# Kernel optimization log

Measured on AMD Instinct MI355X. Metric: run time of the kernel, lower is better.

The kernel has to match this reference:

```python
import jax, jax.numpy as jnp
import numpy as np

N_NODES = 10000
N_EDGES = 320000
D_NODE = 128
D_EDGE = 32
D_IN = 2 * D_NODE + D_EDGE  # 288, concat(sender, receiver, edge)
D_HID = 192                 # AutoMLP log-spaced hidden dim between 288 and 128
D_OUT = 128


def setup_inputs() -> dict:
    key = jax.random.key(0)
    ks = jax.random.split(key, 8)
    n_embed = jax.random.normal(ks[0], (N_NODES, D_NODE), dtype=jnp.float32)
    e_embed = jax.random.normal(ks[1], (N_EDGES, D_EDGE), dtype=jnp.float32)
    senders = jnp.sort(jax.random.randint(ks[2], (N_EDGES,), 0, N_NODES, dtype=jnp.int32))
    receivers = jax.random.randint(ks[3], (N_EDGES,), 0, N_NODES, dtype=jnp.int32)
    # AutoMLP parameters (lecun_normal-style scaling)
    W1 = jax.random.normal(ks[4], (D_IN, D_HID), dtype=jnp.float32) / np.sqrt(D_IN)
    b1 = jnp.zeros((D_HID,), dtype=jnp.float32)
    W2 = jax.random.normal(ks[5], (D_HID, D_OUT), dtype=jnp.float32) / np.sqrt(D_HID)
    b2 = jnp.zeros((D_OUT,), dtype=jnp.float32)
    return {"n_embed": n_embed, "e_embed": e_embed, "senders": senders,
            "receivers": receivers, "W1": W1, "b1": b1, "W2": W2, "b2": b2}


def reference(n_embed, e_embed, senders, receivers, W1, b1, W2, b2):
    # gather sender/receiver node embeddings and concat with edge features: [E, 288]
    inp = jnp.concatenate([n_embed[senders], n_embed[receivers], e_embed], axis=-1)
    # AutoMLP: Dense -> tanh -> Dense (final layer linear)
    h = jnp.tanh(inp @ W1 + b1)          # [E, 192]
    msg = h @ W2 + b2                    # [E, 128]
    # segment_mean over senders (sorted), num_segments = n_nodes
    seg_sum = jax.ops.segment_sum(msg, senders, num_segments=N_NODES,
                                  indices_are_sorted=True)
    counts = jax.ops.segment_sum(jnp.ones((msg.shape[0],), dtype=msg.dtype), senders,
                                 num_segments=N_NODES, indices_are_sorted=True)
    return seg_sum / jnp.maximum(counts, 1.0)[:, None]
```

## Files before the change

kernel.cpp:

```cpp
#include <hip/hip_runtime.h>

#define E_TOT 320000
#define NN    10000
#define DN    128
#define DE    32
#define DH    192
#define DO    128
#define EB    64
#define SHS   196

typedef __attribute__((ext_vector_type(8))) short bf16x8;
typedef __attribute__((ext_vector_type(4))) float f32x4;

#define W1_FRAGS (8*12*64)
#define E_FRAGS  (12*64)
#define W2_FRAGS (6*8*64)
#define FRAGS_TOT (W1_FRAGS + E_FRAGS + W2_FRAGS)
#define ZH (NN * DH / 4)
__device__ __align__(16) unsigned short g_p1[W1_FRAGS * 8];
__device__ __align__(16) unsigned short g_e [E_FRAGS * 8];
__device__ __align__(16) unsigned short g_p2[W2_FRAGS * 8];

__device__ __forceinline__ unsigned short f2bf(float f) {
    union { float f; unsigned u; } v; v.f = f;
    return (unsigned short)((v.u + 0x7FFFu + ((v.u >> 16) & 1u)) >> 16);
}
__device__ __forceinline__ float bflo(unsigned u) {
    union { unsigned v; float f; } t; t.v = u << 16; return t.f;
}
__device__ __forceinline__ float bfhi(unsigned u) {
    union { unsigned v; float f; } t; t.v = u & 0xFFFF0000u; return t.f;
}
__device__ __forceinline__ float bf2f(unsigned short s) {
    union { unsigned v; float f; } t; t.v = (unsigned)s << 16; return t.f;
}
__device__ __forceinline__ float tanh_fast(float x) {
    float ex = __expf(x + x);
    return 1.0f - 2.0f * __builtin_amdgcn_rcpf(ex + 1.0f);
}
__device__ __forceinline__ unsigned cvt_pk_bf16(float lo, float hi) {
    unsigned r;
    asm("v_cvt_pk_bf16_f32 %0, %1, %2" : "=v"(r) : "v"(lo), "v"(hi));
    return r;
}

__global__ void prep(const float* __restrict__ W1, const float* __restrict__ W2,
                     const int* __restrict__ senders,
                     float* __restrict__ Hbar, int* __restrict__ row_start)
{
    int f = blockIdx.x * 256 + threadIdx.x;
    unsigned short tmp[8];
    if (f < W1_FRAGS) {
        int kk = f / (12 * 64), nt = (f >> 6) % 12, lane = f & 63;
        int r0 = kk * 32 + ((lane >> 4) << 3);
        int c  = nt * 16 + (lane & 15);
        #pragma unroll
        for (int i = 0; i < 8; ++i) tmp[i] = f2bf(W1[(r0 + i) * DH + c]);
        *(uint4*)(g_p1 + (size_t)f * 8) = *(const uint4*)tmp;
    } else if (f < W1_FRAGS + E_FRAGS) {
        int f2 = f - W1_FRAGS;
        int mt = f2 >> 6, lane = f2 & 63;
        int k0 = ((lane >> 4) << 3);
        int hid = mt * 16 + (lane & 15);
        #pragma unroll
        for (int i = 0; i < 8; ++i) tmp[i] = f2bf(W1[(256 + k0 + i) * DH + hid]);
        *(uint4*)(g_e + (size_t)f2 * 8) = *(const uint4*)tmp;
    } else if (f < FRAGS_TOT) {
        int f3 = f - W1_FRAGS - E_FRAGS;
        int kk = f3 / (8 * 64), nt = (f3 >> 6) % 8, lane = f3 & 63;
        int r0 = kk * 32 + ((lane >> 4) << 3);
        int c  = nt * 16 + (lane & 15);
        #pragma unroll
        for (int i = 0; i < 8; ++i) tmp[i] = f2bf(W2[(r0 + i) * DO + c]);
        *(uint4*)(g_p2 + (size_t)f3 * 8) = *(const uint4*)tmp;
    } else if (f < FRAGS_TOT + ZH) {
        ((float4*)Hbar)[f - FRAGS_TOT] = make_float4(0.f, 0.f, 0.f, 0.f);
    } else if (f < FRAGS_TOT + ZH + E_TOT) {
        int e = f - FRAGS_TOT - ZH;
        int s_cur  = senders[e];
        int s_prev = (e == 0) ? -1 : senders[e - 1];
        if (s_prev != s_cur)
            for (int n = s_prev + 1; n <= s_cur; ++n) row_start[n] = e;
        if (e == E_TOT - 1)
            for (int n = s_cur + 1; n <= NN; ++n) row_start[n] = E_TOT;
    }
}

__global__ __launch_bounds__(256) void node_proj(
    const float* __restrict__ n_embed, const float* __restrict__ b1,
    unsigned short* __restrict__ P)
{
    __shared__ __align__(16) unsigned short s_a[64][136];
    const int tid  = threadIdx.x;
    const int half = blockIdx.y;
    const int n0   = blockIdx.x * 64;

    #pragma unroll
    for (int it = 0; it < 8; ++it) {
        int idx = tid + it * 256;
        int row = idx >> 5, c = idx & 31;
        float4 v = make_float4(0.f, 0.f, 0.f, 0.f);
        if (n0 + row < NN) v = ((const float4*)(n_embed + (size_t)(n0 + row) * DN))[c];
        unsigned t0 = cvt_pk_bf16(v.x, v.y), t1 = cvt_pk_bf16(v.z, v.w);
        *(uint2*)&s_a[row][c * 4] = make_uint2(t0, t1);
    }
    __syncthreads();

    const int lane = tid & 63, w = tid >> 6;
    const int arow = lane & 15, akb = (lane >> 4) * 8, rbase = (lane >> 4) * 4;

    f32x4 acc[4][3];
    #pragma unroll
    for (int mt = 0; mt < 4; ++mt)
        #pragma unroll
        for (int j = 0; j < 3; ++j) acc[mt][j] = (f32x4){0.f, 0.f, 0.f, 0.f};

    for (int kk = 0; kk < 4; ++kk) {
        bf16x8 a[4], b[3];
        #pragma unroll
        for (int mt = 0; mt < 4; ++mt)
            a[mt] = *(const bf16x8*)&s_a[mt * 16 + arow][kk * 32 + akb];
        #pragma unroll
        for (int j = 0; j < 3; ++j)
            b[j] = *(const bf16x8*)(g_p1 + (((size_t)(kk + 4 * half) * 12 + (3 * w + j)) * 64 + lane) * 8);
        #pragma unroll
        for (int mt = 0; mt < 4; ++mt)
            #pragma unroll
            for (int j = 0; j < 3; ++j)
                acc[mt][j] = __builtin_amdgcn_mfma_f32_16x16x32_bf16(a[mt], b[j], acc[mt][j], 0, 0, 0);
    }

    unsigned short* Pout = P + (size_t)half * NN * DH;
    float bj[3];
    #pragma unroll
    for (int j = 0; j < 3; ++j) bj[j] = (half == 0) ? b1[48 * w + 16 * j + arow] : 0.f;
    const int gq = arow >> 2, ii = arow & 3;
    #pragma unroll
    for (int mt = 0; mt < 4; ++mt)
        #pragma unroll
        for (int j = 0; j < 3; ++j)
            #pragma unroll
            for (int r = 0; r < 4; ++r) {
                int row = n0 + mt * 16 + rbase + r;
                if (row < NN)
                    Pout[((size_t)row * 4 + gq) * 48 + (3 * w + j) * 4 + ii] =
                        f2bf(acc[mt][j][r] + bj[j]);
            }
}

__global__ __launch_bounds__(256) void edge_reduce(
    const float* __restrict__ e_embed,
    const int* __restrict__ senders, const int* __restrict__ receivers,
    const unsigned short* __restrict__ Ps, const unsigned short* __restrict__ Pr,
    float* __restrict__ Hbar)
{
    __shared__ __align__(16) unsigned short s_h[EB][SHS];
    __shared__ int s_send[EB];

    const int tid  = threadIdx.x;
    const int nb8  = gridDim.x >> 3;
    const int e0   = (((blockIdx.x & 7) * nb8) + (blockIdx.x >> 3)) * EB;
    const int lane = tid & 63, w = tid >> 6;
    const int arow = lane & 15, g = lane >> 4;

    const int myedge = e0 + w * 16 + arow;
    const int sN = senders[myedge], rN = receivers[myedge];
    const unsigned short* psbase = Ps + ((size_t)sN * 4 + g) * 48;
    const unsigned short* prbase = Pr + ((size_t)rN * 4 + g) * 48;
    uint4 psq[6], prq[6];
    #pragma unroll
    for (int j = 0; j < 6; ++j) {
        psq[j] = *(const uint4*)(psbase + j * 8);
        prq[j] = *(const uint4*)(prbase + j * 8);
    }
    union { bf16x8 v; unsigned u[4]; } bfr;
    {
        const float* erow = e_embed + (size_t)myedge * DE + g * 8;
        float4 ev0 = *(const float4*)erow;
        float4 ev1 = *(const float4*)(erow + 4);
        bfr.u[0] = cvt_pk_bf16(ev0.x, ev0.y);
        bfr.u[1] = cvt_pk_bf16(ev0.z, ev0.w);
        bfr.u[2] = cvt_pk_bf16(ev1.x, ev1.y);
        bfr.u[3] = cvt_pk_bf16(ev1.z, ev1.w);
    }
    if (tid < EB) s_send[tid] = senders[e0 + tid];

    #pragma unroll
    for (int mt = 0; mt < 12; ++mt) {
        unsigned px, py, qx, qy;
        if ((mt & 1) == 0) {
            px = psq[mt >> 1].x; py = psq[mt >> 1].y;
            qx = prq[mt >> 1].x; qy = prq[mt >> 1].y;
        } else {
            px = psq[mt >> 1].z; py = psq[mt >> 1].w;
            qx = prq[mt >> 1].z; qy = prq[mt >> 1].w;
        }
        f32x4 cinit;
        cinit[0] = bflo(px) + bflo(qx);
        cinit[1] = bfhi(px) + bfhi(qx);
        cinit[2] = bflo(py) + bflo(qy);
        cinit[3] = bfhi(py) + bfhi(qy);
        bf16x8 af = *(const bf16x8*)(g_e + ((size_t)mt * 64 + lane) * 8);
        f32x4 acc = __builtin_amdgcn_mfma_f32_16x16x32_bf16(af, bfr.v, cinit, 0, 0, 0);
        float t0 = tanh_fast(acc[0]);
        float t1 = tanh_fast(acc[1]);
        float t2 = tanh_fast(acc[2]);
        float t3 = tanh_fast(acc[3]);
        *(uint2*)&s_h[w * 16 + arow][mt * 16 + g * 4] =
            make_uint2(cvt_pk_bf16(t0, t1), cvt_pk_bf16(t2, t3));
    }
    __syncthreads();

    if (tid < DH) {
        const int c = tid;
        float sum = 0.f;
        int cur = s_send[0];
        #pragma unroll 8
        for (int e = 0; e < EB; ++e) {
            sum += bf2f(s_h[e][c]);
            int nxt = (e + 1 < EB) ? s_send[e + 1] : -1;
            if (nxt != cur) {
                atomicAdd(&Hbar[(size_t)cur * DH + c], sum);
                sum = 0.f;
                cur = nxt;
            }
        }
    }
}

__global__ __launch_bounds__(256) void node_out(
    const float* __restrict__ Hbar, const int* __restrict__ row_start,
    const float* __restrict__ b2, float* __restrict__ out)
{
    const int tid  = threadIdx.x;
    const int lane = tid & 63, w = tid >> 6;
    const int n0   = (blockIdx.x * 4 + w) * 16;
    if (n0 >= NN) return;
    const int arow = lane & 15, akb = (lane >> 4) * 8, rbase = (lane >> 4) * 4;

    const int myrow = (n0 + arow < NN) ? (n0 + arow) : (NN - 1);
    const int cnt = row_start[myrow + 1] - row_start[myrow];
    const float ic = (cnt > 0) ? 1.0f / (float)cnt : 0.0f;

    const float* hrow = Hbar + (size_t)myrow * DH;
    union { bf16x8 v; unsigned u[4]; } a[6];
    #pragma unroll
    for (int kk = 0; kk < 6; ++kk) {
        float4 v0 = *(const float4*)(hrow + kk * 32 + akb);
        float4 v1 = *(const float4*)(hrow + kk * 32 + akb + 4);
        a[kk].u[0] = cvt_pk_bf16(v0.x * ic, v0.y * ic);
        a[kk].u[1] = cvt_pk_bf16(v0.z * ic, v0.w * ic);
        a[kk].u[2] = cvt_pk_bf16(v1.x * ic, v1.y * ic);
        a[kk].u[3] = cvt_pk_bf16(v1.z * ic, v1.w * ic);
    }

    f32x4 acc[8];
    #pragma unroll
    for (int j = 0; j < 8; ++j) acc[j] = (f32x4){0.f, 0.f, 0.f, 0.f};

    #pragma unroll
    for (int kk = 0; kk < 6; ++kk)
        #pragma unroll
        for (int j = 0; j < 8; ++j) {
            bf16x8 b = *(const bf16x8*)(g_p2 + (((size_t)kk * 8 + j) * 64 + lane) * 8);
            acc[j] = __builtin_amdgcn_mfma_f32_16x16x32_bf16(a[kk].v, b, acc[j], 0, 0, 0);
        }

    #pragma unroll
    for (int j = 0; j < 8; ++j) {
        const float bd = b2[j * 16 + arow];
        #pragma unroll
        for (int r = 0; r < 4; ++r) {
            int row = n0 + rbase + r;
            if (row < NN)
                out[(size_t)row * DO + j * 16 + arow] = acc[j][r] + bd;
        }
    }
}

extern "C" void kernel_launch(void* const* d_in, const int* in_sizes, int n_in,
                              void* d_out, int out_size, void* d_ws, size_t ws_size,
                              hipStream_t stream)
{
    const float* n_embed   = (const float*)d_in[0];
    const float* e_embed   = (const float*)d_in[1];
    const int*   senders   = (const int*)d_in[2];
    const int*   receivers = (const int*)d_in[3];
    const float* W1        = (const float*)d_in[4];
    const float* b1        = (const float*)d_in[5];
    const float* W2        = (const float*)d_in[6];
    const float* b2        = (const float*)d_in[7];
    float* out = (float*)d_out;

    unsigned short* Ps   = (unsigned short*)d_ws;
    unsigned short* Pr   = Ps + (size_t)NN * DH;
    float*          Hbar = (float*)(Pr + (size_t)NN * DH);
    int*            row_start = (int*)(Hbar + (size_t)NN * DH);

    const int prep_items = FRAGS_TOT + ZH + E_TOT;
    prep<<<(prep_items + 255) / 256, 256, 0, stream>>>(W1, W2, senders, Hbar, row_start);
    node_proj<<<dim3((NN + 63) / 64, 2), 256, 0, stream>>>(n_embed, b1, Ps);
    edge_reduce<<<E_TOT / EB, 256, 0, stream>>>(
        e_embed, senders, receivers, Ps, Pr, Hbar);
    node_out<<<(NN + 63) / 64, 256, 0, stream>>>(Hbar, row_start, b2, out);
}
```

Before: 79.23 us.

## Segment-reduce edge hidden states via MFMA with one-hot run matrix

Replaces the serial per-column scan over 64 edges, which used only 192 of 256 threads, with a matrix-core reduction. Hidden activations are stored transposed in LDS, and a wave ballot computes sender run ids. Each run group is then summed by multiplying against a one-hot bf16 matrix with MFMA, and the partial sums are atomically added to Hbar. This costs scattered 2-byte transposed LDS stores, which may cause bank conflicts, plus a per-lane one-hot build.

```diff
diff --git a/kernel.cpp b/kernel.cpp
--- a/kernel.cpp
+++ b/kernel.cpp
@@ -7,7 +7,7 @@
 #define DH    192
 #define DO    128
 #define EB    64
-#define SHS   196
+#define SHT   72
 
 typedef __attribute__((ext_vector_type(8))) short bf16x8;
 typedef __attribute__((ext_vector_type(4))) float f32x4;
@@ -30,9 +30,6 @@
 }
 __device__ __forceinline__ float bfhi(unsigned u) {
     union { unsigned v; float f; } t; t.v = u & 0xFFFF0000u; return t.f;
-}
-__device__ __forceinline__ float bf2f(unsigned short s) {
-    union { unsigned v; float f; } t; t.v = (unsigned)s << 16; return t.f;
 }
 __device__ __forceinline__ float tanh_fast(float x) {
     float ex = __expf(x + x);
@@ -154,8 +151,11 @@
     const unsigned short* __restrict__ Ps, const unsigned short* __restrict__ Pr,
     float* __restrict__ Hbar)
 {
-    __shared__ __align__(16) unsigned short s_h[EB][SHS];
+    __shared__ __align__(16) unsigned short s_hT[DH][SHT];
     __shared__ int s_send[EB];
+    __shared__ int s_runid[EB];
+    __shared__ int s_runnode[EB];
+    __shared__ int s_nruns;
 
     const int tid  = threadIdx.x;
     const int nb8  = gridDim.x >> 3;
@@ -184,6 +184,18 @@
         bfr.u[3] = cvt_pk_bf16(ev1.z, ev1.w);
     }
     if (tid < EB) s_send[tid] = senders[e0 + tid];
+
+    if (w == 0) {
+        int e = lane;
+        int cur  = s_send[e];
+        int prev = (e == 0) ? -1 : s_send[e - 1];
+        bool bnd = (prev != cur);
+        unsigned long long mask = __ballot(bnd);
+        int rid = __popcll(mask << (63 - e)) - 1;
+        s_runid[e] = rid;
+        if (bnd) s_runnode[rid] = cur;
+        if (e == 63) s_nruns = rid + 1;
+    }
 
     #pragma unroll
     for (int mt = 0; mt < 12; ++mt) {
@@ -202,27 +214,48 @@
         cinit[3] = bfhi(py) + bfhi(qy);
         bf16x8 af = *(const bf16x8*)(g_e + ((size_t)mt * 64 + lane) * 8);
         f32x4 acc = __builtin_amdgcn_mfma_f32_16x16x32_bf16(af, bfr.v, cinit, 0, 0, 0);
-        float t0 = tanh_fast(acc[0]);
-        float t1 = tanh_fast(acc[1]);
-        float t2 = tanh_fast(acc[2]);
-        float t3 = tanh_fast(acc[3]);
-        *(uint2*)&s_h[w * 16 + arow][mt * 16 + g * 4] =
-            make_uint2(cvt_pk_bf16(t0, t1), cvt_pk_bf16(t2, t3));
+        unsigned u01 = cvt_pk_bf16(tanh_fast(acc[0]), tanh_fast(acc[1]));
+        unsigned u23 = cvt_pk_bf16(tanh_fast(acc[2]), tanh_fast(acc[3]));
+        const int ecol = w * 16 + arow;
+        s_hT[mt * 16 + g * 4 + 0][ecol] = (unsigned short)(u01 & 0xFFFFu);
+        s_hT[mt * 16 + g * 4 + 1][ecol] = (unsigned short)(u01 >> 16);
+        s_hT[mt * 16 + g * 4 + 2][ecol] = (unsigned short)(u23 & 0xFFFFu);
+        s_hT[mt * 16 + g * 4 + 3][ecol] = (unsigned short)(u23 >> 16);
     }
     __syncthreads();
 
-    if (tid < DH) {
-        const int c = tid;
-        float sum = 0.f;
-        int cur = s_send[0];
-        #pragma unroll 8
-        for (int e = 0; e < EB; ++e) {
-            sum += bf2f(s_h[e][c]);
-            int nxt = (e + 1 < EB) ? s_send[e + 1] : -1;
-            if (nxt != cur) {
-                atomicAdd(&Hbar[(size_t)cur * DH + c], sum);
-                sum = 0.f;
-                cur = nxt;
+    {
+        const int nruns = s_nruns;
+        for (int p = 0; p * 16 < nruns; ++p) {
+            union { bf16x8 v; unsigned u[4]; } bfrag[2];
+            #pragma unroll
+            for (int kh = 0; kh < 2; ++kh)
+                #pragma unroll
+                for (int ii = 0; ii < 4; ++ii) {
+                    int k0 = kh * 32 + g * 8 + ii * 2;
+                    unsigned lo = (s_runid[k0]     == p * 16 + arow) ? 0x3F80u : 0u;
+                    unsigned hi = (s_runid[k0 + 1] == p * 16 + arow) ? 0x3F80u : 0u;
+                    bfrag[kh].u[ii] = lo | (hi << 16);
+                }
+            const int run16 = p * 16 + arow;
+            const bool act  = run16 < nruns;
+            const int node  = act ? s_runnode[run16] : 0;
+            #pragma unroll
+            for (int m = 0; m < 3; ++m) {
+                const int mt = w * 3 + m;
+                f32x4 acc = (f32x4){0.f, 0.f, 0.f, 0.f};
+                #pragma unroll
+                for (int kh = 0; kh < 2; ++kh) {
+                    bf16x8 a = *(const bf16x8*)&s_hT[mt * 16 + arow][kh * 32 + g * 8];
+                    acc = __builtin_amdgcn_mfma_f32_16x16x32_bf16(a, bfrag[kh].v, acc, 0, 0, 0);
+                }
+                if (act) {
+                    float* hb = &Hbar[(size_t)node * DH + mt * 16 + g * 4];
+                    atomicAdd(hb + 0, acc[0]);
+                    atomicAdd(hb + 1, acc[1]);
+                    atomicAdd(hb + 2, acc[2]);
+                    atomicAdd(hb + 3, acc[3]);
+                }
             }
         }
     }
```

Measured after the change: 85.60 us. +8.0%, slower.
